# Kernel tuning notes

Measured on AMD Instinct MI355X. Metric: run time of the kernel, lower is better.

## Reference

```python
import jax, jax.numpy as jnp
import numpy as np

N, E, C, L, B = 40000, 640000, 128, 3, 64
EPS = 1e-5


def _layer_norm(h, g, b):
    m = h.mean(-1, keepdims=True)
    v = h.var(-1, keepdims=True)
    return (h - m) / jnp.sqrt(v + EPS) * g + b


def setup_inputs() -> dict:
    key = jax.random.key(0)
    ks = jax.random.split(key, 24)
    s = 0.05
    inp = {
        "x": jax.random.normal(ks[0], (N, C), jnp.float32),
        "edge_index": jax.random.randint(ks[1], (2, E), 0, N, dtype=jnp.int32),
        "batch": jnp.sort(jax.random.randint(ks[2], (N,), 0, B, dtype=jnp.int32)),
        # pre-scaler Linear(in=C -> hidden=C)
        "pre_w": jax.random.normal(ks[3], (C, C), jnp.float32) * s,
        "pre_b": jnp.zeros((C,), jnp.float32),
        # per-layer GCNConv weight/bias
        "conv_w": jax.random.normal(ks[4], (L, C, C), jnp.float32) * s,
        "conv_b": jnp.zeros((L, C), jnp.float32),
        # per-layer post-conv LayerNorm (applied for layers 0..L-2)
        "ln_g": jnp.ones((L, C), jnp.float32),
        "ln_b": jnp.zeros((L, C), jnp.float32),
        # per-layer FFN: lin1, lin2, LayerNorm
        "ffn_w1": jax.random.normal(ks[5], (L, C, C), jnp.float32) * s,
        "ffn_b1": jnp.zeros((L, C), jnp.float32),
        "ffn_w2": jax.random.normal(ks[6], (L, C, C), jnp.float32) * s,
        "ffn_b2": jnp.zeros((L, C), jnp.float32),
        "ffn_ln_g": jnp.ones((L, C), jnp.float32),
        "ffn_ln_b": jnp.zeros((L, C), jnp.float32),
        # classifier MLP: Linear(C,C)+ReLU+Linear(C,1)
        "cls_w1": jax.random.normal(ks[7], (C, C), jnp.float32) * s,
        "cls_b1": jnp.zeros((C,), jnp.float32),
        "cls_w2": jax.random.normal(ks[8], (C, 1), jnp.float32) * s,
        "cls_b2": jnp.zeros((1,), jnp.float32),
    }
    return inp


def reference(x, edge_index, batch, pre_w, pre_b, conv_w, conv_b, ln_g, ln_b,
              ffn_w1, ffn_b1, ffn_w2, ffn_b2, ffn_ln_g, ffn_ln_b,
              cls_w1, cls_b1, cls_w2, cls_b2):
    src, dst = edge_index[0], edge_index[1]
    # GCN symmetric normalization with self-loops: deg counts incoming edges + 1
    deg = jax.ops.segment_sum(jnp.ones((E,), x.dtype), dst, num_segments=N) + 1.0
    inv_sqrt = jax.lax.rsqrt(deg)                      # [N]
    norm_e = inv_sqrt[src] * inv_sqrt[dst]             # [E]
    self_norm = inv_sqrt * inv_sqrt                    # [N], 1/deg for self-loop

    h = x @ pre_w + pre_b                              # pre_scaler

    for i in range(L):
        layer_in = h
        hw = h @ conv_w[i]                             # [N,C]
        msg = hw[src] * norm_e[:, None]                # gather + scale [E,C]
        h = jax.ops.segment_sum(msg, dst, num_segments=N)
        h = h + hw * self_norm[:, None] + conv_b[i]    # self-loop + bias
        if i < L - 1:
            h = _layer_norm(h, ln_g[i], ln_b[i])       # norm
            h = jax.nn.relu(h)                         # act (act_first=False)
            h = h + layer_in                           # residual (dropout=0)
            # FFN: lin2(relu(lin1(h))) + h, then norm
            y = jax.nn.relu(h @ ffn_w1[i] + ffn_b1[i]) @ ffn_w2[i] + ffn_b2[i] + h
            h = _layer_norm(y, ffn_ln_g[i], ffn_ln_b[i])

    # global mean pool per graph
    counts = jax.ops.segment_sum(jnp.ones((N,), h.dtype), batch, num_segments=B)
    g = jax.ops.segment_sum(h, batch, num_segments=B) / jnp.maximum(counts, 1.0)[:, None]

    out = jax.nn.relu(g @ cls_w1 + cls_b1) @ cls_w2 + cls_b2   # [B,1]
    return out
```

## Files before the change

kernel.cpp:

```cpp
#include <hip/hip_runtime.h>
#include <hip/hip_fp16.h>
#include <cstdint>
#include <cstddef>

#define N_NODES 40000
#define N_EDGES 640000
#define CH 128
#define NL 3
#define NB 64
#define LN_EPS 1e-5f
#define TSTRIDE 132

typedef short short8 __attribute__((ext_vector_type(8)));
typedef float floatx4 __attribute__((ext_vector_type(4)));

__device__ __forceinline__ unsigned short bf16_rne(float f) {
    unsigned int u = __float_as_uint(f);
    unsigned int r = u + 0x7FFF + ((u >> 16) & 1);
    return (unsigned short)(r >> 16);
}


__global__ void deg_kernel(const int* __restrict__ ei, int* __restrict__ degi) {
    int e = blockIdx.x * 256 + threadIdx.x;
    if (e < N_EDGES) atomicAdd(&degi[ei[N_EDGES + e]], 1);
}

__global__ void scan1_kernel(const int* __restrict__ degi, int* __restrict__ rowptr,
                             int* __restrict__ bsum, float* __restrict__ isq) {
    __shared__ int s[256];
    int t = threadIdx.x;
    int i = blockIdx.x * 256 + t;
    int v = (i < N_NODES) ? degi[i] : 0;
    if (i < N_NODES) isq[i] = rsqrtf((float)v + 1.0f);
    s[t] = v;
    __syncthreads();
    for (int off = 1; off < 256; off <<= 1) {
        int add = (t >= off) ? s[t - off] : 0;
        __syncthreads();
        s[t] += add;
        __syncthreads();
    }
    if (i < N_NODES) rowptr[i + 1] = s[t];
    if (t == 255) bsum[blockIdx.x] = s[255];
}

__global__ void scan2_kernel(int* __restrict__ bsum, int* __restrict__ boff, int nb) {
    __shared__ int s[256];
    int t = threadIdx.x;
    int v = (t < nb) ? bsum[t] : 0;
    s[t] = v;
    __syncthreads();
    for (int off = 1; off < 256; off <<= 1) {
        int add = (t >= off) ? s[t - off] : 0;
        __syncthreads();
        s[t] += add;
        __syncthreads();
    }
    if (t < nb) boff[t] = s[t] - v;
}

__global__ void scan3_kernel(int* __restrict__ rowptr, const int* __restrict__ boff) {
    int i = blockIdx.x * 256 + threadIdx.x;
    if (i < N_NODES) rowptr[i + 1] += boff[blockIdx.x];
    if (i == 0 && blockIdx.x == 0) rowptr[0] = 0;
}

__global__ void fill_csr_kernel(const int* __restrict__ ei, const int* __restrict__ rowptr,
                                int* __restrict__ fill, int* __restrict__ srcs) {
    int e = blockIdx.x * 256 + threadIdx.x;
    if (e < N_EDGES) {
        int s = ei[e];
        int d = ei[N_EDGES + e];
        int pos = atomicAdd(&fill[d], 1);
        srcs[rowptr[d] + pos] = s;
    }
}

__global__ void pack_w_kernel(const float* __restrict__ pre_w, const float* __restrict__ conv_w,
                              const float* __restrict__ ffn_w1, const float* __restrict__ ffn_w2,
                              short* __restrict__ wpk) {
    int idx = blockIdx.x * 256 + threadIdx.x;
    int mat = idx >> 14;
    int e = idx & 16383;
    int k = e >> 7, n = e & 127;
    const float* src;
    switch (mat) {
        case 0: src = pre_w; break;
        case 1: case 2: case 3: src = conv_w + (size_t)(mat - 1) * 16384; break;
        case 4: case 5: src = ffn_w1 + (size_t)(mat - 4) * 16384; break;
        default: src = ffn_w2 + (size_t)(mat - 6) * 16384; break;
    }
    float f = src[e];
    unsigned short h = bf16_rne(f);
    float hf = __uint_as_float((unsigned)h << 16);
    unsigned short l = bf16_rne(f - hf);
    int kk = k >> 5, quad = (k >> 3) & 3, j = k & 7;
    int frag = ((kk * 4 + quad) * 128 + n) * 8 + j;
    wpk[(size_t)mat * 32768 + frag] = (short)h;
    wpk[(size_t)mat * 32768 + 16384 + frag] = (short)l;
}


__device__ __forceinline__ void gld_lds16(const short* g, short* l) {
    __builtin_amdgcn_global_load_lds(
        (const __attribute__((address_space(1))) unsigned int*)g,
        (__attribute__((address_space(3))) unsigned int*)l, 16, 0, 0);
}

template <int VARIANT>
__launch_bounds__(256, 2)
__global__ void gemm_fused(const float* __restrict__ A, const short* __restrict__ W1pk,
                           const float* __restrict__ b1, const short* __restrict__ W2pk,
                           const float* __restrict__ b2, const float* __restrict__ Res,
                           const float* __restrict__ gamma, const float* __restrict__ beta,
                           const short* __restrict__ W3pk,
                           float* __restrict__ OutG, __half* __restrict__ OutC) {
    __shared__ short wsm[16384];
    __shared__ float tbuf[64 * TSTRIDE];
    const int tid = threadIdx.x;
    const int lane = tid & 63;
    const int wv = tid >> 6;
    const int row0 = blockIdx.x * 64 + wv * 16;
    const int m = lane & 15;
    const int quad = lane >> 4;

    floatx4 acc[8];
#pragma unroll
    for (int c = 0; c < 8; ++c) acc[c] = (floatx4){0.f, 0.f, 0.f, 0.f};

    const float* arow = A + (size_t)(row0 + m) * CH + quad * 8;
    float* trow_w = tbuf + (wv * 16) * TSTRIDE;
    const float* trow = tbuf + (wv * 16 + m) * TSTRIDE + quad * 8;

#pragma unroll 1
    for (int h = 0; h < 2; ++h) {
#pragma unroll
        for (int r = 0; r < 4; ++r) {
            int off = r * 2048 + tid * 8;
            gld_lds16(W1pk + h * 8192 + off, wsm + off);
        }
#pragma unroll
        for (int r = 0; r < 4; ++r) {
            int off = r * 2048 + tid * 8;
            gld_lds16(W1pk + 16384 + h * 8192 + off, wsm + 8192 + off);
        }
        __syncthreads();

#pragma unroll 1
        for (int kx = 0; kx < 2; ++kx) {
            const int kk = h * 2 + kx;
            float4 a0 = *(const float4*)(arow + kk * 32);
            float4 a1 = *(const float4*)(arow + kk * 32 + 4);
            float av[8] = {a0.x, a0.y, a0.z, a0.w, a1.x, a1.y, a1.z, a1.w};
            short8 ahi, alo;
#pragma unroll
            for (int j = 0; j < 8; ++j) {
                unsigned short hb = bf16_rne(av[j]);
                ahi[j] = (short)hb;
                alo[j] = (short)bf16_rne(av[j] - __uint_as_float((unsigned)hb << 16));
            }
            const short* sm_h = wsm + ((kx * 4 + quad) * 128 + m) * 8;
            const short* sm_l = sm_h + 8192;
#pragma unroll
            for (int c = 0; c < 8; ++c) {
                short8 bhi = *(const short8*)(sm_h + c * 128);
                short8 blo = *(const short8*)(sm_l + c * 128);
                acc[c] = __builtin_amdgcn_mfma_f32_16x16x32_bf16(ahi, bhi, acc[c], 0, 0, 0);
                acc[c] = __builtin_amdgcn_mfma_f32_16x16x32_bf16(alo, bhi, acc[c], 0, 0, 0);
                acc[c] = __builtin_amdgcn_mfma_f32_16x16x32_bf16(ahi, blo, acc[c], 0, 0, 0);
            }
        }
        __syncthreads();
    }

#pragma unroll
    for (int c = 0; c < 8; ++c) {
        int col = c * 16 + m;
        float bv = b1[col];
#pragma unroll
        for (int r = 0; r < 4; ++r) {
            int lrow = quad * 4 + r;
            float v = acc[c][r] + bv;
            if (VARIANT == 1) v = fmaxf(v, 0.f);
            trow_w[lrow * TSTRIDE + col] = v;
            if (VARIANT == 0)
                OutG[(size_t)(row0 + quad * 4 + r) * CH + col] = v;
        }
        acc[c] = (floatx4){0.f, 0.f, 0.f, 0.f};
    }

#pragma unroll 1
    for (int h = 0; h < 2; ++h) {
#pragma unroll
        for (int r = 0; r < 4; ++r) {
            int off = r * 2048 + tid * 8;
            gld_lds16(W2pk + h * 8192 + off, wsm + off);
        }
#pragma unroll
        for (int r = 0; r < 4; ++r) {
            int off = r * 2048 + tid * 8;
            gld_lds16(W2pk + 16384 + h * 8192 + off, wsm + 8192 + off);
        }
        __syncthreads();

#pragma unroll 1
        for (int kx = 0; kx < 2; ++kx) {
            const int kk = h * 2 + kx;
            float av[8];
#pragma unroll
            for (int j = 0; j < 8; ++j) av[j] = trow[kk * 32 + j];
            short8 ahi, alo;
#pragma unroll
            for (int j = 0; j < 8; ++j) {
                unsigned short hb = bf16_rne(av[j]);
                ahi[j] = (short)hb;
                alo[j] = (short)bf16_rne(av[j] - __uint_as_float((unsigned)hb << 16));
            }
            const short* sm_h = wsm + ((kx * 4 + quad) * 128 + m) * 8;
            const short* sm_l = sm_h + 8192;
#pragma unroll
            for (int c = 0; c < 8; ++c) {
                short8 bhi = *(const short8*)(sm_h + c * 128);
                short8 blo = *(const short8*)(sm_l + c * 128);
                acc[c] = __builtin_amdgcn_mfma_f32_16x16x32_bf16(ahi, bhi, acc[c], 0, 0, 0);
                acc[c] = __builtin_amdgcn_mfma_f32_16x16x32_bf16(alo, bhi, acc[c], 0, 0, 0);
                acc[c] = __builtin_amdgcn_mfma_f32_16x16x32_bf16(ahi, blo, acc[c], 0, 0, 0);
            }
        }
        __syncthreads();
    }

    if (VARIANT == 0) {
#pragma unroll
        for (int c = 0; c < 8; ++c) {
            int col = c * 16 + m;
#pragma unroll
            for (int r = 0; r < 4; ++r) {
                int row = row0 + quad * 4 + r;
                OutC[(size_t)row * CH + col] = __float2half(acc[c][r]);
            }
        }
        return;
    }

#pragma unroll
    for (int c = 0; c < 8; ++c) {
        int col = c * 16 + m;
        float bv = b2[col];
#pragma unroll
        for (int r = 0; r < 4; ++r)
            acc[c][r] += bv + Res[(size_t)(row0 + quad * 4 + r) * CH + col];
    }
#pragma unroll
    for (int r = 0; r < 4; ++r) {
        float s = 0.f, q = 0.f;
#pragma unroll
        for (int c = 0; c < 8; ++c) {
            float t = acc[c][r];
            s += t;
            q = fmaf(t, t, q);
        }
#pragma unroll
        for (int msk = 1; msk < 16; msk <<= 1) {
            s += __shfl_xor(s, msk);
            q += __shfl_xor(q, msk);
        }
        float mean = s * (1.f / CH);
        float var = q * (1.f / CH) - mean * mean;
        float rstd = rsqrtf(var + LN_EPS);
        int row = row0 + quad * 4 + r;
        int lrow = quad * 4 + r;
#pragma unroll
        for (int c = 0; c < 8; ++c) {
            int col = c * 16 + m;
            float y = (acc[c][r] - mean) * rstd * gamma[col] + beta[col];
            OutG[(size_t)row * CH + col] = y;
            trow_w[lrow * TSTRIDE + col] = y;
        }
    }
#pragma unroll
    for (int c = 0; c < 8; ++c) acc[c] = (floatx4){0.f, 0.f, 0.f, 0.f};

#pragma unroll 1
    for (int h = 0; h < 2; ++h) {
#pragma unroll
        for (int r = 0; r < 4; ++r) {
            int off = r * 2048 + tid * 8;
            gld_lds16(W3pk + h * 8192 + off, wsm + off);
        }
#pragma unroll
        for (int r = 0; r < 4; ++r) {
            int off = r * 2048 + tid * 8;
            gld_lds16(W3pk + 16384 + h * 8192 + off, wsm + 8192 + off);
        }
        __syncthreads();

#pragma unroll 1
        for (int kx = 0; kx < 2; ++kx) {
            const int kk = h * 2 + kx;
            float av[8];
#pragma unroll
            for (int j = 0; j < 8; ++j) av[j] = trow[kk * 32 + j];
            short8 ahi, alo;
#pragma unroll
            for (int j = 0; j < 8; ++j) {
                unsigned short hb = bf16_rne(av[j]);
                ahi[j] = (short)hb;
                alo[j] = (short)bf16_rne(av[j] - __uint_as_float((unsigned)hb << 16));
            }
            const short* sm_h = wsm + ((kx * 4 + quad) * 128 + m) * 8;
            const short* sm_l = sm_h + 8192;
#pragma unroll
            for (int c = 0; c < 8; ++c) {
                short8 bhi = *(const short8*)(sm_h + c * 128);
                short8 blo = *(const short8*)(sm_l + c * 128);
                acc[c] = __builtin_amdgcn_mfma_f32_16x16x32_bf16(ahi, bhi, acc[c], 0, 0, 0);
                acc[c] = __builtin_amdgcn_mfma_f32_16x16x32_bf16(alo, bhi, acc[c], 0, 0, 0);
                acc[c] = __builtin_amdgcn_mfma_f32_16x16x32_bf16(ahi, blo, acc[c], 0, 0, 0);
            }
        }
        __syncthreads();
    }

#pragma unroll
    for (int c = 0; c < 8; ++c) {
        int col = c * 16 + m;
#pragma unroll
        for (int r = 0; r < 4; ++r) {
            int row = row0 + quad * 4 + r;
            OutC[(size_t)row * CH + col] = __float2half(acc[c][r]);
        }
    }
}

template <int FUSED>
__launch_bounds__(256)
__global__ void agg_kernel(const __half* __restrict__ HW, const int* __restrict__ rowptr,
                           const int* __restrict__ srcs, const float* __restrict__ isq,
                           const float* __restrict__ bias, const float* __restrict__ gamma,
                           const float* __restrict__ beta, float* __restrict__ Hres,
                           float* __restrict__ Out) {
    const int lane = threadIdx.x & 63;
    const int node = blockIdx.x * 4 + (threadIdx.x >> 6);
    const int start = rowptr[node];
    const int end = rowptr[node + 1];

    float ax = 0.f, ay = 0.f;
    for (int base = start; base < end; base += 64) {
        int idx = base + lane;
        int clamped = (idx < end) ? idx : (end - 1);
        int sl = srcs[clamped];
        float wl = isq[sl];
        int cnt = end - base;
        if (cnt > 64) cnt = 64;
        int j = 0;
        for (; j + 8 <= cnt; j += 8) {
            int s[8];
            float w[8];
            float2 v[8];
#pragma unroll
            for (int q = 0; q < 8; ++q) {
                s[q] = __shfl(sl, j + q);
                w[q] = __shfl(wl, j + q);
            }
#pragma unroll
            for (int q = 0; q < 8; ++q)
                v[q] = __half22float2(*(const __half2*)(HW + (size_t)s[q] * CH + lane * 2));
#pragma unroll
            for (int q = 0; q < 8; ++q) {
                ax = fmaf(w[q], v[q].x, ax);
                ay = fmaf(w[q], v[q].y, ay);
            }
        }
        for (; j + 4 <= cnt; j += 4) {
            int s0 = __shfl(sl, j), s1 = __shfl(sl, j + 1);
            int s2 = __shfl(sl, j + 2), s3 = __shfl(sl, j + 3);
            float w0 = __shfl(wl, j), w1 = __shfl(wl, j + 1);
            float w2 = __shfl(wl, j + 2), w3 = __shfl(wl, j + 3);
            float2 v0 = __half22float2(*(const __half2*)(HW + (size_t)s0 * CH + lane * 2));
            float2 v1 = __half22float2(*(const __half2*)(HW + (size_t)s1 * CH + lane * 2));
            float2 v2 = __half22float2(*(const __half2*)(HW + (size_t)s2 * CH + lane * 2));
            float2 v3 = __half22float2(*(const __half2*)(HW + (size_t)s3 * CH + lane * 2));
            ax = fmaf(w0, v0.x, ax); ay = fmaf(w0, v0.y, ay);
            ax = fmaf(w1, v1.x, ax); ay = fmaf(w1, v1.y, ay);
            ax = fmaf(w2, v2.x, ax); ay = fmaf(w2, v2.y, ay);
            ax = fmaf(w3, v3.x, ax); ay = fmaf(w3, v3.y, ay);
        }
        for (; j < cnt; ++j) {
            int s = __shfl(sl, j);
            float w = __shfl(wl, j);
            float2 vf = __half22float2(*(const __half2*)(HW + (size_t)s * CH + lane * 2));
            ax = fmaf(w, vf.x, ax);
            ay = fmaf(w, vf.y, ay);
        }
    }
    float d = isq[node];
    const __half2 hv = *(const __half2*)(HW + (size_t)node * CH + lane * 2);
    float2 hf = __half22float2(hv);
    const float2 bb = *(const float2*)(bias + lane * 2);
    float hx = d * ax + d * d * hf.x + bb.x;
    float hy = d * ay + d * d * hf.y + bb.y;

    if (!FUSED) {
        float2 o; o.x = hx; o.y = hy;
        *(float2*)(Out + (size_t)node * CH + lane * 2) = o;
        return;
    }
    float sum = hx + hy;
    float sq = hx * hx + hy * hy;
    for (int msk = 1; msk < 64; msk <<= 1) {
        sum += __shfl_xor(sum, msk);
        sq += __shfl_xor(sq, msk);
    }
    float mean = sum * (1.f / CH);
    float var = sq * (1.f / CH) - mean * mean;
    float rstd = rsqrtf(var + LN_EPS);
    const float2 gg = *(const float2*)(gamma + lane * 2);
    const float2 be = *(const float2*)(beta + lane * 2);
    float y0 = (hx - mean) * rstd * gg.x + be.x;
    float y1 = (hy - mean) * rstd * gg.y + be.y;
    float2* hp = (float2*)(Hres + (size_t)node * CH + lane * 2);
    float2 rr = *hp;
    float2 o;
    o.x = fmaxf(y0, 0.f) + rr.x;
    o.y = fmaxf(y1, 0.f) + rr.y;
    *hp = o;
}

__launch_bounds__(256)
__global__ void pool_kernel(const float* __restrict__ H, const int* __restrict__ batch,
                            float* __restrict__ g, float* __restrict__ cntf) {
    const int lane = threadIdx.x & 63;
    const int w = blockIdx.x * 4 + (threadIdx.x >> 6);
    const int n0 = w * 16;
    float lx = 0.f, ly = 0.f;
    int run = 0;
    int cur = batch[n0];
    for (int t = 0; t < 16; ++t) {
        int n = n0 + t;
        int b = batch[n];
        if (b != cur) {
            atomicAdd(&g[(size_t)cur * CH + lane * 2], lx);
            atomicAdd(&g[(size_t)cur * CH + lane * 2 + 1], ly);
            if (lane == 0) atomicAdd(&cntf[cur], (float)run);
            lx = ly = 0.f; run = 0; cur = b;
        }
        const float2 v = *(const float2*)(H + (size_t)n * CH + lane * 2);
        lx += v.x; ly += v.y; ++run;
    }
    atomicAdd(&g[(size_t)cur * CH + lane * 2], lx);
    atomicAdd(&g[(size_t)cur * CH + lane * 2 + 1], ly);
    if (lane == 0) atomicAdd(&cntf[cur], (float)run);
}

__launch_bounds__(128)
__global__ void cls_kernel(const float* __restrict__ g, const float* __restrict__ cntf,
                           const float* __restrict__ w1, const float* __restrict__ b1,
                           const float* __restrict__ w2, const float* __restrict__ b2,
                           float* __restrict__ out) {
    __shared__ float gm[CH];
    __shared__ float red[2];
    const int b = blockIdx.x;
    const int t = threadIdx.x;
    float inv = 1.f / fmaxf(cntf[b], 1.f);
    gm[t] = g[(size_t)b * CH + t] * inv;
    __syncthreads();
    float acc = b1[t];
    for (int k = 0; k < CH; ++k) acc = fmaf(gm[k], w1[(size_t)k * CH + t], acc);
    float v = fmaxf(acc, 0.f) * w2[t];
    for (int msk = 1; msk < 64; msk <<= 1) v += __shfl_xor(v, msk);
    if ((t & 63) == 0) red[t >> 6] = v;
    __syncthreads();
    if (t == 0) out[b] = red[0] + red[1] + b2[0];
}


extern "C" void kernel_launch(void* const* d_in, const int* in_sizes, int n_in,
                              void* d_out, int out_size, void* d_ws, size_t ws_size,
                              hipStream_t stream) {
    const float* x      = (const float*)d_in[0];
    const int*   ei     = (const int*)d_in[1];
    const int*   batch  = (const int*)d_in[2];
    const float* pre_w  = (const float*)d_in[3];
    const float* pre_b  = (const float*)d_in[4];
    const float* conv_w = (const float*)d_in[5];
    const float* conv_b = (const float*)d_in[6];
    const float* ln_g   = (const float*)d_in[7];
    const float* ln_b   = (const float*)d_in[8];
    const float* ffn_w1 = (const float*)d_in[9];
    const float* ffn_b1 = (const float*)d_in[10];
    const float* ffn_w2 = (const float*)d_in[11];
    const float* ffn_b2 = (const float*)d_in[12];
    const float* fln_g  = (const float*)d_in[13];
    const float* fln_b  = (const float*)d_in[14];
    const float* cls_w1 = (const float*)d_in[15];
    const float* cls_b1 = (const float*)d_in[16];
    const float* cls_w2 = (const float*)d_in[17];
    const float* cls_b2 = (const float*)d_in[18];

    float* H    = (float*)d_ws;
    float* T    = H + (size_t)N_NODES * CH;
    float* R    = T + (size_t)N_NODES * CH;
    __half* HWh = (__half*)R;
    int*   degi = (int*)(R + (size_t)N_NODES * CH);
    int*   fill = degi + N_NODES;
    float* g    = (float*)(fill + N_NODES);
    float* cntf = g + (size_t)NB * CH;
    float* isq  = cntf + NB;
    int*  rowptr = (int*)(isq + N_NODES);
    int*  bsum   = rowptr + N_NODES + 1;
    int*  boff   = bsum + 256;
    int*  srcs   = boff + 256;
    short* wpk   = (short*)(srcs + N_EDGES);

    const int nb_scan = (N_NODES + 255) / 256;

    hipMemsetAsync(degi, 0, (size_t)(2 * N_NODES + NB * CH + NB) * sizeof(int), stream);

    deg_kernel<<<N_EDGES / 256, 256, 0, stream>>>(ei, degi);
    scan1_kernel<<<nb_scan, 256, 0, stream>>>(degi, rowptr, bsum, isq);
    scan2_kernel<<<1, 256, 0, stream>>>(bsum, boff, nb_scan);
    scan3_kernel<<<nb_scan, 256, 0, stream>>>(rowptr, boff);
    fill_csr_kernel<<<N_EDGES / 256, 256, 0, stream>>>(ei, rowptr, fill, srcs);
    pack_w_kernel<<<8 * 16384 / 256, 256, 0, stream>>>(pre_w, conv_w, ffn_w1, ffn_w2, wpk);

    const int gblk = N_NODES / 64;
    const int lblk = N_NODES / 4;

    gemm_fused<0><<<gblk, 256, 0, stream>>>(x, wpk, pre_b,
                                            wpk + 1 * 32768, nullptr, nullptr,
                                            nullptr, nullptr, nullptr, H, HWh);

    for (int i = 0; i < NL; ++i) {
        if (i < NL - 1) {
            agg_kernel<1><<<lblk, 256, 0, stream>>>(HWh, rowptr, srcs, isq,
                                                    conv_b + (size_t)i * CH,
                                                    ln_g + (size_t)i * CH,
                                                    ln_b + (size_t)i * CH, H, nullptr);
            gemm_fused<1><<<gblk, 256, 0, stream>>>(H, wpk + (size_t)(4 + i) * 32768,
                                                    ffn_b1 + (size_t)i * CH,
                                                    wpk + (size_t)(6 + i) * 32768,
                                                    ffn_b2 + (size_t)i * CH, H,
                                                    fln_g + (size_t)i * CH,
                                                    fln_b + (size_t)i * CH,
                                                    wpk + (size_t)(2 + i) * 32768,
                                                    H, HWh);
        } else {
            agg_kernel<0><<<lblk, 256, 0, stream>>>(HWh, rowptr, srcs, isq,
                                                    conv_b + (size_t)i * CH,
                                                    nullptr, nullptr, nullptr, T);
        }
    }

    pool_kernel<<<N_NODES / 64, 256, 0, stream>>>(T, batch, g, cntf);
    cls_kernel<<<NB, CH, 0, stream>>>(g, cntf, cls_w1, cls_b1, cls_w2, cls_b2,
                                      (float*)d_out);
}
```

Baseline: 360.9 us.

## Load packed weight fragments directly from global memory instead of staging in LDS

Drops the 32KB shared-memory weight buffer and its global_load_lds staging with block barriers. Each wave now reads its bf16 hi/lo weight fragments straight from global memory (expected to hit in L1/L2), batching all loads before the MFMAs. Freeing LDS and removing the syncthreads allows raising the occupancy hint from 2 to 3 blocks per CU. The cost is redundant global and L2 traffic, since all four waves and every block reload the same weights, and added register pressure from holding 16 short8 fragments.

```diff
diff --git a/kernel.cpp b/kernel.cpp
--- a/kernel.cpp
+++ b/kernel.cpp
@@ -102,21 +102,39 @@
 }
 
 
-__device__ __forceinline__ void gld_lds16(const short* g, short* l) {
-    __builtin_amdgcn_global_load_lds(
-        (const __attribute__((address_space(1))) unsigned int*)g,
-        (__attribute__((address_space(3))) unsigned int*)l, 16, 0, 0);
+__device__ __forceinline__ void split8(const float* av, short8& ahi, short8& alo) {
+#pragma unroll
+    for (int j = 0; j < 8; ++j) {
+        unsigned short hb = bf16_rne(av[j]);
+        ahi[j] = (short)hb;
+        alo[j] = (short)bf16_rne(av[j] - __uint_as_float((unsigned)hb << 16));
+    }
+}
+
+__device__ __forceinline__ void bload_mfma(const short* __restrict__ bh,
+                                           short8 ahi, short8 alo, floatx4* acc) {
+    short8 bhi[8], blo[8];
+#pragma unroll
+    for (int c = 0; c < 8; ++c) {
+        bhi[c] = *(const short8*)(bh + c * 128);
+        blo[c] = *(const short8*)(bh + 16384 + c * 128);
+    }
+#pragma unroll
+    for (int c = 0; c < 8; ++c) {
+        acc[c] = __builtin_amdgcn_mfma_f32_16x16x32_bf16(ahi, bhi[c], acc[c], 0, 0, 0);
+        acc[c] = __builtin_amdgcn_mfma_f32_16x16x32_bf16(alo, bhi[c], acc[c], 0, 0, 0);
+        acc[c] = __builtin_amdgcn_mfma_f32_16x16x32_bf16(ahi, blo[c], acc[c], 0, 0, 0);
+    }
 }
 
 template <int VARIANT>
-__launch_bounds__(256, 2)
+__launch_bounds__(256, 3)
 __global__ void gemm_fused(const float* __restrict__ A, const short* __restrict__ W1pk,
                            const float* __restrict__ b1, const short* __restrict__ W2pk,
                            const float* __restrict__ b2, const float* __restrict__ Res,
                            const float* __restrict__ gamma, const float* __restrict__ beta,
                            const short* __restrict__ W3pk,
                            float* __restrict__ OutG, __half* __restrict__ OutC) {
-    __shared__ short wsm[16384];
     __shared__ float tbuf[64 * TSTRIDE];
     const int tid = threadIdx.x;
     const int lane = tid & 63;
@@ -132,46 +150,16 @@
     const float* arow = A + (size_t)(row0 + m) * CH + quad * 8;
     float* trow_w = tbuf + (wv * 16) * TSTRIDE;
     const float* trow = tbuf + (wv * 16 + m) * TSTRIDE + quad * 8;
+    const int boff = quad * 1024 + m * 8;
 
 #pragma unroll 1
-    for (int h = 0; h < 2; ++h) {
-#pragma unroll
-        for (int r = 0; r < 4; ++r) {
-            int off = r * 2048 + tid * 8;
-            gld_lds16(W1pk + h * 8192 + off, wsm + off);
-        }
-#pragma unroll
-        for (int r = 0; r < 4; ++r) {
-            int off = r * 2048 + tid * 8;
-            gld_lds16(W1pk + 16384 + h * 8192 + off, wsm + 8192 + off);
-        }
-        __syncthreads();
-
-#pragma unroll 1
-        for (int kx = 0; kx < 2; ++kx) {
-            const int kk = h * 2 + kx;
-            float4 a0 = *(const float4*)(arow + kk * 32);
-            float4 a1 = *(const float4*)(arow + kk * 32 + 4);
-            float av[8] = {a0.x, a0.y, a0.z, a0.w, a1.x, a1.y, a1.z, a1.w};
-            short8 ahi, alo;
-#pragma unroll
-            for (int j = 0; j < 8; ++j) {
-                unsigned short hb = bf16_rne(av[j]);
-                ahi[j] = (short)hb;
-                alo[j] = (short)bf16_rne(av[j] - __uint_as_float((unsigned)hb << 16));
-            }
-            const short* sm_h = wsm + ((kx * 4 + quad) * 128 + m) * 8;
-            const short* sm_l = sm_h + 8192;
-#pragma unroll
-            for (int c = 0; c < 8; ++c) {
-                short8 bhi = *(const short8*)(sm_h + c * 128);
-                short8 blo = *(const short8*)(sm_l + c * 128);
-                acc[c] = __builtin_amdgcn_mfma_f32_16x16x32_bf16(ahi, bhi, acc[c], 0, 0, 0);
-                acc[c] = __builtin_amdgcn_mfma_f32_16x16x32_bf16(alo, bhi, acc[c], 0, 0, 0);
-                acc[c] = __builtin_amdgcn_mfma_f32_16x16x32_bf16(ahi, blo, acc[c], 0, 0, 0);
-            }
-        }
-        __syncthreads();
+    for (int kk = 0; kk < 4; ++kk) {
+        float4 a0 = *(const float4*)(arow + kk * 32);
+        float4 a1 = *(const float4*)(arow + kk * 32 + 4);
+        float av[8] = {a0.x, a0.y, a0.z, a0.w, a1.x, a1.y, a1.z, a1.w};
+        short8 ahi, alo;
+        split8(av, ahi, alo);
+        bload_mfma(W1pk + kk * 4096 + boff, ahi, alo, acc);
     }
 
 #pragma unroll
@@ -191,44 +179,13 @@
     }
 
 #pragma unroll 1
-    for (int h = 0; h < 2; ++h) {
-#pragma unroll
-        for (int r = 0; r < 4; ++r) {
-            int off = r * 2048 + tid * 8;
-            gld_lds16(W2pk + h * 8192 + off, wsm + off);
-        }
-#pragma unroll
-        for (int r = 0; r < 4; ++r) {
-            int off = r * 2048 + tid * 8;
-            gld_lds16(W2pk + 16384 + h * 8192 + off, wsm + 8192 + off);
-        }
-        __syncthreads();
-
-#pragma unroll 1
-        for (int kx = 0; kx < 2; ++kx) {
-            const int kk = h * 2 + kx;
-            float av[8];
-#pragma unroll
-            for (int j = 0; j < 8; ++j) av[j] = trow[kk * 32 + j];
-            short8 ahi, alo;
-#pragma unroll
-            for (int j = 0; j < 8; ++j) {
-                unsigned short hb = bf16_rne(av[j]);
-                ahi[j] = (short)hb;
-                alo[j] = (short)bf16_rne(av[j] - __uint_as_float((unsigned)hb << 16));
-            }
-            const short* sm_h = wsm + ((kx * 4 + quad) * 128 + m) * 8;
-            const short* sm_l = sm_h + 8192;
-#pragma unroll
-            for (int c = 0; c < 8; ++c) {
-                short8 bhi = *(const short8*)(sm_h + c * 128);
-                short8 blo = *(const short8*)(sm_l + c * 128);
-                acc[c] = __builtin_amdgcn_mfma_f32_16x16x32_bf16(ahi, bhi, acc[c], 0, 0, 0);
-                acc[c] = __builtin_amdgcn_mfma_f32_16x16x32_bf16(alo, bhi, acc[c], 0, 0, 0);
-                acc[c] = __builtin_amdgcn_mfma_f32_16x16x32_bf16(ahi, blo, acc[c], 0, 0, 0);
-            }
-        }
-        __syncthreads();
+    for (int kk = 0; kk < 4; ++kk) {
+        float4 t0 = *(const float4*)(trow + kk * 32);
+        float4 t1 = *(const float4*)(trow + kk * 32 + 4);
+        float av[8] = {t0.x, t0.y, t0.z, t0.w, t1.x, t1.y, t1.z, t1.w};
+        short8 ahi, alo;
+        split8(av, ahi, alo);
+        bload_mfma(W2pk + kk * 4096 + boff, ahi, alo, acc);
     }
 
     if (VARIANT == 0) {
@@ -283,44 +240,13 @@
     for (int c = 0; c < 8; ++c) acc[c] = (floatx4){0.f, 0.f, 0.f, 0.f};
 
 #pragma unroll 1
-    for (int h = 0; h < 2; ++h) {
-#pragma unroll
-        for (int r = 0; r < 4; ++r) {
-            int off = r * 2048 + tid * 8;
-            gld_lds16(W3pk + h * 8192 + off, wsm + off);
-        }
-#pragma unroll
-        for (int r = 0; r < 4; ++r) {
-            int off = r * 2048 + tid * 8;
-            gld_lds16(W3pk + 16384 + h * 8192 + off, wsm + 8192 + off);
-        }
-        __syncthreads();
-
-#pragma unroll 1
-        for (int kx = 0; kx < 2; ++kx) {
-            const int kk = h * 2 + kx;
-            float av[8];
-#pragma unroll
-            for (int j = 0; j < 8; ++j) av[j] = trow[kk * 32 + j];
-            short8 ahi, alo;
-#pragma unroll
-            for (int j = 0; j < 8; ++j) {
-                unsigned short hb = bf16_rne(av[j]);
-                ahi[j] = (short)hb;
-                alo[j] = (short)bf16_rne(av[j] - __uint_as_float((unsigned)hb << 16));
-            }
-            const short* sm_h = wsm + ((kx * 4 + quad) * 128 + m) * 8;
-            const short* sm_l = sm_h + 8192;
-#pragma unroll
-            for (int c = 0; c < 8; ++c) {
-                short8 bhi = *(const short8*)(sm_h + c * 128);
-                short8 blo = *(const short8*)(sm_l + c * 128);
-                acc[c] = __builtin_amdgcn_mfma_f32_16x16x32_bf16(ahi, bhi, acc[c], 0, 0, 0);
-                acc[c] = __builtin_amdgcn_mfma_f32_16x16x32_bf16(alo, bhi, acc[c], 0, 0, 0);
-                acc[c] = __builtin_amdgcn_mfma_f32_16x16x32_bf16(ahi, blo, acc[c], 0, 0, 0);
-            }
-        }
-        __syncthreads();
+    for (int kk = 0; kk < 4; ++kk) {
+        float4 t0 = *(const float4*)(trow + kk * 32);
+        float4 t1 = *(const float4*)(trow + kk * 32 + 4);
+        float av[8] = {t0.x, t0.y, t0.z, t0.w, t1.x, t1.y, t1.z, t1.w};
+        short8 ahi, alo;
+        split8(av, ahi, alo);
+        bload_mfma(W3pk + kk * 4096 + boff, ahi, alo, acc);
     }
 
 #pragma unroll
```

Measured after the change: 362.0 us. No clear change (+0.3%).
